# Kernel tuning notes

Measured on AMD Instinct MI355X. Metric: run time of the kernel, lower is better.

The kernel has to match this reference:

```python
import jax, jax.numpy as jnp
import numpy as np

HEADS, DIM_HEAD, BITS = 12, 64, 4


def quantize(q, bits):
    # per-tensor affine fake-quant, exactly as the torch quantize()
    s = (q.max() - q.min()) / (2.0 ** bits - 1.0)
    z = jnp.round(2.0 ** bits - 1.0 - q.max() / s)
    return jnp.round(q / s + z), s, z


def setup_inputs() -> dict:
    key = jax.random.key(0)
    k1, k2, k3, k4 = jax.random.split(key, 4)
    return {
        "x": jax.random.normal(k1, (4, 1024, 768), jnp.float32),
        "w_qkv": jax.random.normal(k2, (2304, 768), jnp.float32) * 0.02,  # torch Linear weight [out,in]
        "w_out": jax.random.normal(k3, (768, 768), jnp.float32) * 0.02,
        "b_out": jax.random.normal(k4, (768,), jnp.float32) * 0.02,
    }


def reference(x, w_qkv, w_out, b_out):
    scale = DIM_HEAD ** -0.5
    B, N, D = x.shape
    # --- quantized QKV projection: x @ W^T with zero-point correction ---
    xq, sx1, zx1 = quantize(x, BITS)
    w1, sw1, zw1 = quantize(w_qkv.T, BITS)  # [D, 3*inner]
    xqkv = (xq @ w1
            - w1.sum(0, keepdims=True) * zx1
            - xq.sum(2, keepdims=True) * zw1
            + zx1 * zw1 * D) * (sx1 * sw1)  # [B, N, 3*inner]
    q, k, v = jnp.split(xqkv, 3, axis=-1)
    to_heads = lambda t: t.reshape(B, N, HEADS, DIM_HEAD).transpose(0, 2, 1, 3)  # b h n d
    q, k, v = to_heads(q), to_heads(k), to_heads(v)
    # --- quantized QK^T (note: original omits the +zq*zk*d term) ---
    qq, sq, zq = quantize(q, BITS)
    kq, sk, zk = quantize(k.transpose(0, 1, 3, 2), BITS)  # b h d n
    dots = (qq @ kq
            - kq.sum(2, keepdims=True) * zq
            - qq.sum(3, keepdims=True) * zk) * (scale * sq * sk)  # b h n n
    a = jax.nn.softmax(dots, axis=-1)
    # --- quantized A @ V ---
    aq, sa, za = quantize(a, BITS)
    vq, sv, zv = quantize(v, BITS)
    out = (aq @ vq
           - vq.sum(2, keepdims=True) * za
           - aq.sum(3, keepdims=True) * zv
           + za * zv * N) * (sa * sv)  # b h n d
    out = out.transpose(0, 2, 1, 3).reshape(B, N, HEADS * DIM_HEAD)
    # --- quantized output projection (faithful to original: correction uses
    # xqkv.sum / xqkv width, reproducing the source's use of `x` here) ---
    oq, sx2, zx2 = quantize(out, BITS)
    w2, sw2, zw2 = quantize(w_out.T, BITS)  # [inner, D]
    o = (oq @ w2
         - w2.sum(0, keepdims=True) * zx2
         - xqkv.sum(2, keepdims=True) * zw2
         + zx2 * zw2 * xqkv.shape[2]) * (sx2 * sw2) + b_out
    return o
```

## Files before the change

kernel.cpp:

```cpp
#include <hip/hip_runtime.h>
#include <math.h>

#define HEADS 12
#define DH    64
#define Dm    768
#define I3    2304
#define Nn    1024
#define Mm    4096
#define BHt   48
#define LOG2E 1.4426950408889634f

#define P_X  0
#define P_W1 1
#define P_Q  2
#define P_K  3
#define P_V  4
#define P_A  5
#define P_O  6
#define P_W2 7

typedef int   v4i __attribute__((ext_vector_type(4)));
typedef float v4f __attribute__((ext_vector_type(4)));

#if __has_builtin(__builtin_amdgcn_exp2f)
#define EXP2(x) __builtin_amdgcn_exp2f(x)
#else
#define EXP2(x) exp2f(x)
#endif

__device__ inline unsigned encf(float f) {
    unsigned u = __float_as_uint(f);
    return (u & 0x80000000u) ? ~u : (u | 0x80000000u);
}
__device__ inline float decf(unsigned u) {
    return (u & 0x80000000u) ? __uint_as_float(u & 0x7fffffffu) : __uint_as_float(~u);
}
__device__ inline void get_sz(const unsigned* scal, int pair, float* s, float* z) {
    float mn = decf(scal[2 * pair]);
    float mx = decf(scal[2 * pair + 1]);
    float ss = (mx - mn) / 15.0f;
    *s = ss;
    *z = rintf(15.0f - mx / ss);
}

__device__ inline void swz_bh(int blk, int* bh, int* itile) {
    int xcd = blk & 7, idx = blk >> 3;
    *itile = idx & 15;
    *bh = xcd + 8 * (idx >> 4);
}

__global__ __launch_bounds__(256) void k_init(unsigned* scal, float* z1, int n1, float* z2, int n2) {
    int g = blockIdx.x * 256 + threadIdx.x;
    if (g < n1) z1[g] = 0.f;
    if (g < n2) z2[g] = 0.f;
    if (g < 8) { scal[2 * g] = 0xFFFFFFFFu; scal[2 * g + 1] = 0u; }
}

__global__ __launch_bounds__(256) void k_minmax3(const float* x, const float* w1, const float* w2,
                                                 unsigned* scal) {
    __shared__ float rmn[256], rmx[256];
    int bid = blockIdx.x, tid = threadIdx.x;
    const float* src; int rows, pair, b0, nb;
    if (bid < 256)      { src = x;  rows = 4096; pair = P_X;  b0 = 0;   nb = 256; }
    else if (bid < 384) { src = w1; rows = 2304; pair = P_W1; b0 = 256; nb = 128; }
    else                { src = w2; rows = 768;  pair = P_W2; b0 = 384; nb = 64;  }
    float mn = INFINITY, mx = -INFINITY;
    for (int r = bid - b0; r < rows; r += nb) {
        const float* row = src + (long)r * 768;
#pragma unroll
        for (int k = 0; k < 3; ++k) {
            float v = row[tid + k * 256];
            mn = fminf(mn, v); mx = fmaxf(mx, v);
        }
    }
    rmn[tid] = mn; rmx[tid] = mx; __syncthreads();
    for (int s = 128; s > 0; s >>= 1) {
        if (tid < s) { rmn[tid] = fminf(rmn[tid], rmn[tid + s]); rmx[tid] = fmaxf(rmx[tid], rmx[tid + s]); }
        __syncthreads();
    }
    if (tid == 0) {
        atomicMin(&scal[2 * pair], encf(rmn[0]));
        atomicMax(&scal[2 * pair + 1], encf(rmx[0]));
    }
}

__global__ __launch_bounds__(256) void k_quant3(const float* x, const float* w1, const float* w2,
                                                const unsigned* scal,
                                                signed char* xq, signed char* wq, signed char* w2q,
                                                float* rs_x, float* rs_w1, float* rs_w2) {
    __shared__ float red[256];
    int bid = blockIdx.x, tid = threadIdx.x;
    const float* src; signed char* dq; float* rs; int pair, r;
    if (bid < 4096)      { src = x;  dq = xq;  rs = rs_x;  pair = P_X;  r = bid; }
    else if (bid < 6400) { src = w1; dq = wq;  rs = rs_w1; pair = P_W1; r = bid - 4096; }
    else                 { src = w2; dq = w2q; rs = rs_w2; pair = P_W2; r = bid - 6400; }
    float s, z; get_sz(scal, pair, &s, &z);
    const float* row = src + (long)r * 768;
    signed char* drow = dq + (long)r * 768;
    float acc = 0.f;
#pragma unroll
    for (int k = 0; k < 3; ++k) {
        int c = tid + k * 256;
        float q = rintf(row[c] / s + z);
        drow[c] = (signed char)(int)q;
        acc += q;
    }
    red[tid] = acc; __syncthreads();
    for (int s2 = 128; s2 > 0; s2 >>= 1) { if (tid < s2) red[tid] += red[tid + s2]; __syncthreads(); }
    if (tid == 0) rs[r] = red[0];
}

__global__ __launch_bounds__(256) void k_quant_rows(const float* src, const unsigned* scal, int pair,
                                                    signed char* dq) {
    int r = blockIdx.x, tid = threadIdx.x;
    float s, z; get_sz(scal, pair, &s, &z);
    const float* row = src + (long)r * 768;
    signed char* drow = dq + (long)r * 768;
#pragma unroll
    for (int k = 0; k < 3; ++k) {
        int c = tid + k * 256;
        float q = rintf(row[c] / s + z);
        drow[c] = (signed char)(int)q;
    }
}

__global__ __launch_bounds__(256) void k_gemm_mfma(const signed char* A, const signed char* B,
                                                   const float* colsumB, const float* rowsumA,
                                                   const float* bias, float* C, int K, int ldC,
                                                   const unsigned* scal, int pairA, int pairB,
                                                   float corrK, int do_stats, float* rowsum_out,
                                                   unsigned* scal_mm) {
    __shared__ __align__(16) signed char As[128 * 64];
    __shared__ __align__(16) signed char Bs[128 * 64];
    __shared__ float red[256];
    int tid = threadIdx.x;
    int wave = tid >> 6, lane = tid & 63;
    int col16 = lane & 15, quad = lane >> 4;
    long rowbase = (long)blockIdx.y * 128;
    long colbase = (long)blockIdx.x * 128;

    int c4 = tid & 3, r4 = tid >> 2;
    const signed char* ag0 = A + (rowbase + r4) * K + c4 * 16;
    const signed char* ag1 = A + (rowbase + r4 + 64) * K + c4 * 16;
    const signed char* bg0 = B + (colbase + r4) * K + c4 * 16;
    const signed char* bg1 = B + (colbase + r4 + 64) * K + c4 * 16;
    int soff0 = ((r4 >> 4) << 10) + (c4 << 8) + ((r4 & 15) << 4);
    int soff1 = soff0 + 4096;

    v4i ra0 = *(const v4i*)ag0;
    v4i ra1 = *(const v4i*)ag1;
    v4i rb0 = *(const v4i*)bg0;
    v4i rb1 = *(const v4i*)bg1;

    const int afrag_off = wave * 2048 + quad * 256 + col16 * 16;
    const int bfrag_off = quad * 256 + col16 * 16;
    v4i acc[2][8] = {};
    int nk = K >> 6;
    for (int kt = 0; kt < nk; ++kt) {
        *(v4i*)(As + soff0) = ra0;
        *(v4i*)(As + soff1) = ra1;
        *(v4i*)(Bs + soff0) = rb0;
        *(v4i*)(Bs + soff1) = rb1;
        __syncthreads();
        if (kt + 1 < nk) {
            int ko = (kt + 1) << 6;
            ra0 = *(const v4i*)(ag0 + ko);
            ra1 = *(const v4i*)(ag1 + ko);
            rb0 = *(const v4i*)(bg0 + ko);
            rb1 = *(const v4i*)(bg1 + ko);
        }
        v4i af0 = *(const v4i*)(As + afrag_off);
        v4i af1 = *(const v4i*)(As + afrag_off + 1024);
        v4i bf[8];
#pragma unroll
        for (int g = 0; g < 8; ++g) bf[g] = *(const v4i*)(Bs + bfrag_off + g * 1024);
#pragma unroll
        for (int g = 0; g < 8; ++g) {
            acc[0][g] = __builtin_amdgcn_mfma_i32_16x16x64_i8(af0, bf[g], acc[0][g], 0, 0, 0);
            acc[1][g] = __builtin_amdgcn_mfma_i32_16x16x64_i8(af1, bf[g], acc[1][g], 0, 0, 0);
        }
        __syncthreads();
    }

    float sA, zA, sB, zB;
    get_sz(scal, pairA, &sA, &zA);
    get_sz(scal, pairB, &sB, &zB);
    float sAB = sA * sB;
    float zz = (zA * zB) * corrK;
    float vmn = INFINITY, vmx = -INFINITY;
    float rowpart[2][4] = {};
#pragma unroll
    for (int i2 = 0; i2 < 2; ++i2)
#pragma unroll
        for (int g = 0; g < 8; ++g) {
            long col = colbase + g * 16 + col16;
            float cs = colsumB[col] * zA;
            float bv = bias ? bias[col] : 0.f;
#pragma unroll
            for (int r = 0; r < 4; ++r) {
                long row = rowbase + wave * 32 + i2 * 16 + quad * 4 + r;
                float v = ((float)acc[i2][g][r] - cs - rowsumA[row] * zB + zz) * sAB + bv;
                C[row * ldC + col] = v;
                rowpart[i2][r] += v;
                vmn = fminf(vmn, v); vmx = fmaxf(vmx, v);
            }
        }
    if (do_stats) {
#pragma unroll
        for (int i2 = 0; i2 < 2; ++i2)
#pragma unroll
            for (int r = 0; r < 4; ++r) {
                float s = rowpart[i2][r];
                s += __shfl_xor(s, 1); s += __shfl_xor(s, 2);
                s += __shfl_xor(s, 4); s += __shfl_xor(s, 8);
                if (col16 == 0)
                    atomicAdd(&rowsum_out[rowbase + wave * 32 + i2 * 16 + quad * 4 + r], s);
            }
        int pair = P_Q + (int)(colbase / 768);
        red[tid] = vmx; __syncthreads();
        for (int s = 128; s > 0; s >>= 1) { if (tid < s) red[tid] = fmaxf(red[tid], red[tid + s]); __syncthreads(); }
        if (tid == 0) atomicMax(&scal_mm[2 * pair + 1], encf(red[0]));
        __syncthreads();
        red[tid] = vmn; __syncthreads();
        for (int s = 128; s > 0; s >>= 1) { if (tid < s) red[tid] = fminf(red[tid], red[tid + s]); __syncthreads(); }
        if (tid == 0) atomicMin(&scal_mm[2 * pair], encf(red[0]));
    }
}

__global__ __launch_bounds__(256) void k_quant_qkv2(const float* xqkv, const unsigned* scal,
                                                    signed char* qq, signed char* kq, signed char* vqT,
                                                    float* rowsum_qq, float* cskc, float* colsum_vq) {
    __shared__ __align__(16) signed char vt[64 * 80];
    __shared__ float vred[4][64];
    int blk = blockIdx.x;
    int bh = blk >> 4, itile = blk & 15;
    int tid = threadIdx.x;
    int wave = tid >> 6, d = tid & 63;
    int b = bh / HEADS, h = bh - HEADS * b;
    float sq, zq, sk, zk, sv, zv;
    get_sz(scal, P_Q, &sq, &zq);
    get_sz(scal, P_K, &sk, &zk);
    get_sz(scal, P_V, &sv, &zv);
    float zqcsc2 = zq * ((0.125f * sq) * sk) * LOG2E;
    int vb = 0;
    float vsum = 0.f;
    for (int ir = 0; ir < 16; ++ir) {
        int il = wave * 16 + ir;
        int i = itile * 64 + il;
        const float* row = xqkv + ((long)b * Nn + i) * I3 + h * DH;
        float q = rintf(row[d] / sq + zq);
        float k = rintf(row[768 + d] / sk + zk);
        float v = rintf(row[1536 + d] / sv + zv);
        long o = ((long)bh * Nn + i) * 64 + d;
        qq[o] = (signed char)(int)q;
        kq[o] = (signed char)(int)k;
        vsum += v;
        vb |= ((int)v & 0xff) << ((ir & 3) * 8);
        if ((ir & 3) == 3) {
            *(int*)(vt + d * 80 + (il & ~3)) = vb;
            vb = 0;
        }
        float s1 = q, s2 = k;
        for (int off = 32; off > 0; off >>= 1) {
            s1 += __shfl_down(s1, off);
            s2 += __shfl_down(s2, off);
        }
        if (d == 0) { rowsum_qq[bh * Nn + i] = s1; cskc[bh * Nn + i] = s2 * zqcsc2; }
    }
    vred[wave][d] = vsum;
    __syncthreads();
    int dd = tid >> 2, c = tid & 3;
    *(v4i*)(vqT + ((long)bh * 64 + dd) * 1024 + itile * 64 + c * 16) = *(const v4i*)(vt + dd * 80 + c * 16);
    if (tid < 64)
        atomicAdd(&colsum_vq[bh * 64 + tid],
                  ((vred[0][tid] + vred[1][tid]) + vred[2][tid]) + vred[3][tid]);
}

__global__ __launch_bounds__(256) void k_attn_a8(const signed char* qq, const signed char* kq,
                                                 const float* rowsum_qq, const float* cskc,
                                                 unsigned* scal, float* rowmax, float* sumexp) {
    __shared__ float red[256];
    int bh, itile;
    swz_bh(blockIdx.x, &bh, &itile);
    int tid = threadIdx.x;
    int wave = tid >> 6, lane = tid & 63;
    int col16 = lane & 15, quad = lane >> 4;
    int rowbase = itile * 64 + wave * 16;
    const signed char* kbase = kq + (long)bh * Nn * 64;
    v4i qfrag = *(const v4i*)(qq + ((long)bh * Nn + rowbase + col16) * 64 + quad * 16);
    float sq, zq, sk, zk;
    get_sz(scal, P_Q, &sq, &zq);
    get_sz(scal, P_K, &sk, &zk);
    float csc2 = ((0.125f * sq) * sk) * LOG2E;
    int irow = bh * Nn + rowbase + col16;
    float roff = rowsum_qq[irow] * zk * csc2;
    v4i zero = {0, 0, 0, 0};
    float m[4]    = {-INFINITY, -INFINITY, -INFINITY, -INFINITY};
    float se[4]   = {0.f, 0.f, 0.f, 0.f};
    float lmin[4] = {INFINITY, INFINITY, INFINITY, INFINITY};
    const signed char* kf = kbase + (long)col16 * 64 + quad * 16;
    const float* ckq = cskc + bh * Nn + quad * 4;
    v4i kb[2][4];
#pragma unroll
    for (int t = 0; t < 4; ++t)
        kb[0][t] = *(const v4i*)(kf + (long)(t * 16) * 64);
#pragma unroll 2
    for (int ch = 0; ch < 16; ++ch) {
        int cur = ch & 1, nxt = cur ^ 1;
        int pch = (ch < 15) ? ch + 1 : 15;
#pragma unroll
        for (int t = 0; t < 4; ++t)
            kb[nxt][t] = *(const v4i*)(kf + (long)(pch * 64 + t * 16) * 64);
#pragma unroll
        for (int s = 0; s < 4; ++s) {
            v4i d = __builtin_amdgcn_mfma_i32_16x16x64_i8(kb[cur][s], qfrag, zero, 0, 0, 0);
            v4f ck4 = *(const v4f*)(ckq + ch * 64 + s * 16);
#pragma unroll
            for (int r = 0; r < 4; ++r) {
                float dv = fmaf((float)d[r], csc2, -(ck4[r] + roff));
                lmin[r] = fminf(lmin[r], dv);
                float mn = fmaxf(m[r], dv);
                float e = EXP2(fminf(m[r], dv) - mn);
                se[r] = (dv > m[r]) ? fmaf(se[r], e, 1.0f) : (se[r] + e);
                m[r] = mn;
            }
        }
    }
    float mm = fmaxf(fmaxf(m[0], m[1]), fmaxf(m[2], m[3]));
    float seT = fmaf(se[0], EXP2(m[0] - mm),
               fmaf(se[1], EXP2(m[1] - mm),
               fmaf(se[2], EXP2(m[2] - mm), se[3] * EXP2(m[3] - mm))));
    float lmT = fminf(fminf(lmin[0], lmin[1]), fminf(lmin[2], lmin[3]));
#pragma unroll
    for (int off = 16; off <= 32; off <<= 1) {
        float mo = __shfl_xor(mm, off);
        float so = __shfl_xor(seT, off);
        float lo = __shfl_xor(lmT, off);
        float mn = fmaxf(mm, mo);
        seT = fmaf(seT, EXP2(mm - mn), so * EXP2(mo - mn));
        mm = mn;
        lmT = fminf(lmT, lo);
    }
    if (quad == 0) {
        rowmax[irow] = mm;
        sumexp[irow] = seT;
    }
    float amax_c = 1.0f / seT;
    float amin_c = EXP2(lmT - mm) / seT;
    red[tid] = amax_c; __syncthreads();
    for (int s = 128; s > 0; s >>= 1) { if (tid < s) red[tid] = fmaxf(red[tid], red[tid + s]); __syncthreads(); }
    if (tid == 0) atomicMax(&scal[2 * P_A + 1], encf(red[0]));
    __syncthreads();
    red[tid] = amin_c; __syncthreads();
    for (int s = 128; s > 0; s >>= 1) { if (tid < s) red[tid] = fminf(red[tid], red[tid + s]); __syncthreads(); }
    if (tid == 0) atomicMin(&scal[2 * P_A], encf(red[0]));
}

__global__ __launch_bounds__(256) void k_attn_b8(const signed char* qq, const signed char* kq,
                                                 const signed char* vqT, const float* rowsum_qq,
                                                 const float* cskc, const float* colsum_vq,
                                                 const float* rowmax, const float* sumexp,
                                                 unsigned* scal, float* out_mat) {
    __shared__ __align__(16) signed char AqB[8192];
    __shared__ float red[256];
    int bh, itile;
    swz_bh(blockIdx.x, &bh, &itile);
    int tid = threadIdx.x;
    int wave = tid >> 6, lane = tid & 63;
    int col16 = lane & 15, quad = lane >> 4;
    int rowbase = itile * 64 + wave * 16;
    int b = bh / HEADS, h = bh - HEADS * b;
    const signed char* kbase = kq + (long)bh * Nn * 64;
    const signed char* vbase = vqT + (long)bh * 64 * 1024;
    v4i qfrag = *(const v4i*)(qq + ((long)bh * Nn + rowbase + col16) * 64 + quad * 16);
    float sq, zq, sk, zk, sv, zv, sa, za;
    get_sz(scal, P_Q, &sq, &zq);
    get_sz(scal, P_K, &sk, &zk);
    get_sz(scal, P_V, &sv, &zv);
    get_sz(scal, P_A, &sa, &za);
    float csc2 = ((0.125f * sq) * sk) * LOG2E;
    int irow = bh * Nn + rowbase + col16;
    float roff = rowsum_qq[irow] * zk * csc2 + rowmax[irow];
    float crcp = 1.0f / (sumexp[irow] * sa);
    v4i accPV[4] = {};
    float rs_a = 0.f;
    v4i zero = {0, 0, 0, 0};
    const signed char* kf = kbase + (long)col16 * 64 + quad * 16;
    const float* ckq = cskc + bh * Nn + quad * 4;
    const int wbase = wave * 1024 + col16 * 16 + quad * 4;
    const int rbase = wave * 1024 + quad * 256 + col16 * 16;

    v4i kb0[4], kb1[4];
#pragma unroll
    for (int t = 0; t < 4; ++t) {
        kb0[t] = *(const v4i*)(kf + (long)(t * 16) * 64);
        kb1[t] = *(const v4i*)(kf + (long)(64 + t * 16) * 64);
    }

#define QUANT_CHUNK(CH, BUF, KB)                                                        \
    {                                                                                   \
        _Pragma("unroll")                                                               \
        for (int s = 0; s < 4; ++s) {                                                   \
            v4i d = __builtin_amdgcn_mfma_i32_16x16x64_i8(KB[s], qfrag, zero, 0, 0, 0); \
            v4f ck4 = *(const v4f*)(ckq + (CH) * 64 + s * 16);                          \
            unsigned pks = 0;                                                           \
            _Pragma("unroll")                                                           \
            for (int r = 0; r < 4; ++r) {                                               \
                float es = fmaf((float)d[r], csc2, -(ck4[r] + roff));                   \
                float aqv = rintf(fmaf(EXP2(es), crcp, za));                            \
                rs_a += aqv;                                                            \
                pks |= ((unsigned)(int)aqv & 255u) << (8 * r);                          \
            }                                                                           \
            *(int*)(AqB + (BUF) * 4096 + wbase + s * 256) = (int)pks;                   \
        }                                                                               \
    }

#define BODY(CH, CUR, KBc, KBn)                                                         \
    {                                                                                   \
        v4i pa = *(const v4i*)(AqB + (CUR) * 4096 + rbase);                             \
        v4i bv[4];                                                                      \
        _Pragma("unroll")                                                               \
        for (int g = 0; g < 4; ++g)                                                     \
            bv[g] = *(const v4i*)(vbase + (long)(g * 16 + col16) * 1024 + (CH) * 64 + quad * 16); \
        if ((CH) < 14) {                                                                \
            _Pragma("unroll")                                                           \
            for (int t = 0; t < 4; ++t)                                                 \
                KBc[t] = *(const v4i*)(kf + (long)(((CH) + 2) * 64 + t * 16) * 64);     \
        }                                                                               \
        if ((CH) < 15) QUANT_CHUNK((CH) + 1, 1 - (CUR), KBn)                            \
        _Pragma("unroll")                                                               \
        for (int g = 0; g < 4; ++g)                                                     \
            accPV[g] = __builtin_amdgcn_mfma_i32_16x16x64_i8(bv[g], pa, accPV[g], 0, 0, 0); \
    }

    QUANT_CHUNK(0, 0, kb0)
    for (int ch2 = 0; ch2 < 8; ++ch2) {
        int ch = ch2 * 2;
        BODY(ch, 0, kb0, kb1)
        BODY(ch + 1, 1, kb1, kb0)
    }
#undef BODY
#undef QUANT_CHUNK

    rs_a += __shfl_xor(rs_a, 16);
    rs_a += __shfl_xor(rs_a, 32);

    float sav = sa * sv;
    float zz = (za * zv) * 1024.0f;
    float vmn = INFINITY, vmx = -INFINITY;
    long obase = ((long)b * Nn + rowbase + col16) * Dm + h * DH;
#pragma unroll
    for (int g = 0; g < 4; ++g) {
        int d4 = g * 16 + quad * 4;
        v4f cs4 = *(const v4f*)(colsum_vq + bh * 64 + d4);
        v4f ov;
#pragma unroll
        for (int rr = 0; rr < 4; ++rr) {
            float v = ((float)accPV[g][rr] - cs4[rr] * za - rs_a * zv + zz) * sav;
            ov[rr] = v;
            vmn = fminf(vmn, v); vmx = fmaxf(vmx, v);
        }
        *(v4f*)(out_mat + obase + d4) = ov;
    }
    red[tid] = vmx; __syncthreads();
    for (int s = 128; s > 0; s >>= 1) { if (tid < s) red[tid] = fmaxf(red[tid], red[tid + s]); __syncthreads(); }
    if (tid == 0) atomicMax(&scal[2 * P_O + 1], encf(red[0]));
    __syncthreads();
    red[tid] = vmn; __syncthreads();
    for (int s = 128; s > 0; s >>= 1) { if (tid < s) red[tid] = fminf(red[tid], red[tid + s]); __syncthreads(); }
    if (tid == 0) atomicMin(&scal[2 * P_O], encf(red[0]));
}

extern "C" void kernel_launch(void* const* d_in, const int* in_sizes, int n_in,
                              void* d_out, int out_size, void* d_ws, size_t ws_size,
                              hipStream_t stream) {
    const float* x     = (const float*)d_in[0];
    const float* w_qkv = (const float*)d_in[1];
    const float* w_out = (const float*)d_in[2];
    const float* b_out = (const float*)d_in[3];

    char* ws = (char*)d_ws;
    size_t off = 0;
    auto alloc = [&](size_t n) -> char* {
        char* p = ws + off;
        off = (off + n + 255) & ~(size_t)255;
        return p;
    };
    unsigned*    scal        = (unsigned*)alloc(64);
    float*       xqkv        = (float*)alloc((size_t)Mm * I3 * 4);
    float*       out_mat     = (float*)alloc((size_t)Mm * Dm * 4);
    signed char* xq          = (signed char*)alloc((size_t)Mm * Dm);
    signed char* wq          = (signed char*)alloc((size_t)I3 * Dm);
    signed char* w2q         = (signed char*)alloc((size_t)Dm * Dm);
    signed char* oq          = (signed char*)alloc((size_t)Mm * Dm);
    signed char* qq          = (signed char*)alloc((size_t)BHt * Nn * DH);
    signed char* kq          = (signed char*)alloc((size_t)BHt * Nn * DH);
    signed char* vqT         = (signed char*)alloc((size_t)BHt * Nn * DH);
    float*       rowsum_xq   = (float*)alloc((size_t)Mm * 4);
    float*       colsum_w1   = (float*)alloc((size_t)I3 * 4);
    float*       colsum_w2   = (float*)alloc((size_t)Dm * 4);
    float*       rowsum_xqkv = (float*)alloc((size_t)Mm * 4);
    float*       rowsum_qq   = (float*)alloc((size_t)BHt * Nn * 4);
    float*       cskc        = (float*)alloc((size_t)BHt * Nn * 4);
    float*       colsum_vq   = (float*)alloc((size_t)BHt * DH * 4);
    float*       rowmax      = (float*)alloc((size_t)BHt * Nn * 4);
    float*       sumexp      = (float*)alloc((size_t)BHt * Nn * 4);

    k_init<<<28, 256, 0, stream>>>(scal, rowsum_xqkv, Mm, colsum_vq, BHt * DH);

    k_minmax3<<<448, 256, 0, stream>>>(x, w_qkv, w_out, scal);
    k_quant3<<<7168, 256, 0, stream>>>(x, w_qkv, w_out, scal, xq, wq, w2q,
                                       rowsum_xq, colsum_w1, colsum_w2);

    {
        dim3 g(I3 / 128, Mm / 128);
        k_gemm_mfma<<<g, 256, 0, stream>>>(xq, wq, colsum_w1, rowsum_xq, nullptr, xqkv,
                                           Dm, I3, scal, P_X, P_W1, 768.0f,
                                           1, rowsum_xqkv, scal);
    }

    k_quant_qkv2<<<BHt * 16, 256, 0, stream>>>(xqkv, scal, qq, kq, vqT,
                                               rowsum_qq, cskc, colsum_vq);

    k_attn_a8<<<BHt * 16, 256, 0, stream>>>(qq, kq, rowsum_qq, cskc, scal, rowmax, sumexp);
    k_attn_b8<<<BHt * 16, 256, 0, stream>>>(qq, kq, vqT, rowsum_qq, cskc, colsum_vq,
                                            rowmax, sumexp, scal, out_mat);

    k_quant_rows<<<Mm, 256, 0, stream>>>(out_mat, scal, P_O, oq);

    {
        dim3 g(Dm / 128, Mm / 128);
        k_gemm_mfma<<<g, 256, 0, stream>>>(oq, w2q, colsum_w2, rowsum_xqkv, b_out, (float*)d_out,
                                           Dm, Dm, scal, P_O, P_W2, 2304.0f,
                                           0, nullptr, nullptr);
    }
}
```

Before: 261.6 us.

## Split attention key range across wave pairs and double the grid

Both attention kernels now cover 32 query rows per block instead of 64. Each pair of waves splits the 1024 keys into two halves, and the partial softmax statistics (max, sum-exp, min) and partial PV accumulators are merged through shared memory. The launch grid doubles to 1536 blocks, giving more parallelism and shorter per-wave loops across the CUs. In exchange it adds extra syncthreads and LDS merge traffic, and each Q fragment is loaded by twice as many blocks.

```diff
diff --git a/kernel.cpp b/kernel.cpp
--- a/kernel.cpp
+++ b/kernel.cpp
@@ -43,10 +43,10 @@
     *z = rintf(15.0f - mx / ss);
 }
 
-__device__ inline void swz_bh(int blk, int* bh, int* itile) {
+__device__ inline void swz_bh32(int blk, int* bh, int* itile) {
     int xcd = blk & 7, idx = blk >> 3;
-    *itile = idx & 15;
-    *bh = xcd + 8 * (idx >> 4);
+    *itile = idx & 31;
+    *bh = xcd + 8 * (idx >> 5);
 }
 
 __global__ __launch_bounds__(256) void k_init(unsigned* scal, float* z1, int n1, float* z2, int n2) {
@@ -280,12 +280,15 @@
                                                  const float* rowsum_qq, const float* cskc,
                                                  unsigned* scal, float* rowmax, float* sumexp) {
     __shared__ float red[256];
+    __shared__ float Mj[2][64], Sj[2][64], Lj[2][64];
     int bh, itile;
-    swz_bh(blockIdx.x, &bh, &itile);
+    swz_bh32(blockIdx.x, &bh, &itile);
     int tid = threadIdx.x;
     int wave = tid >> 6, lane = tid & 63;
     int col16 = lane & 15, quad = lane >> 4;
-    int rowbase = itile * 64 + wave * 16;
+    int rowbase = itile * 32 + (wave >> 1) * 16;
+    int jhalf = wave & 1;
+    int c0 = jhalf * 8;
     const signed char* kbase = kq + (long)bh * Nn * 64;
     v4i qfrag = *(const v4i*)(qq + ((long)bh * Nn + rowbase + col16) * 64 + quad * 16);
     float sq, zq, sk, zk;
@@ -298,16 +301,16 @@
     float m[4]    = {-INFINITY, -INFINITY, -INFINITY, -INFINITY};
     float se[4]   = {0.f, 0.f, 0.f, 0.f};
     float lmin[4] = {INFINITY, INFINITY, INFINITY, INFINITY};
-    const signed char* kf = kbase + (long)col16 * 64 + quad * 16;
-    const float* ckq = cskc + bh * Nn + quad * 4;
+    const signed char* kf = kbase + (long)(c0 * 64 + col16) * 64 + quad * 16;
+    const float* ckq = cskc + bh * Nn + c0 * 64 + quad * 4;
     v4i kb[2][4];
 #pragma unroll
     for (int t = 0; t < 4; ++t)
         kb[0][t] = *(const v4i*)(kf + (long)(t * 16) * 64);
 #pragma unroll 2
-    for (int ch = 0; ch < 16; ++ch) {
+    for (int ch = 0; ch < 8; ++ch) {
         int cur = ch & 1, nxt = cur ^ 1;
-        int pch = (ch < 15) ? ch + 1 : 15;
+        int pch = (ch < 7) ? ch + 1 : 7;
 #pragma unroll
         for (int t = 0; t < 4; ++t)
             kb[nxt][t] = *(const v4i*)(kf + (long)(pch * 64 + t * 16) * 64);
@@ -341,12 +344,23 @@
         mm = mn;
         lmT = fminf(lmT, lo);
     }
-    if (quad == 0) {
-        rowmax[irow] = mm;
-        sumexp[irow] = seT;
-    }
-    float amax_c = 1.0f / seT;
-    float amin_c = EXP2(lmT - mm) / seT;
+    if (jhalf) { Mj[wave >> 1][lane] = mm; Sj[wave >> 1][lane] = seT; Lj[wave >> 1][lane] = lmT; }
+    __syncthreads();
+    float amax_c = -INFINITY, amin_c = INFINITY;
+    if (!jhalf) {
+        int p = wave >> 1;
+        float m2 = Mj[p][lane], s2 = Sj[p][lane], l2 = Lj[p][lane];
+        float mn = fmaxf(mm, m2);
+        seT = fmaf(seT, EXP2(mm - mn), s2 * EXP2(m2 - mn));
+        mm = mn;
+        lmT = fminf(lmT, l2);
+        if (quad == 0) {
+            rowmax[irow] = mm;
+            sumexp[irow] = seT;
+        }
+        amax_c = 1.0f / seT;
+        amin_c = EXP2(lmT - mm) / seT;
+    }
     red[tid] = amax_c; __syncthreads();
     for (int s = 128; s > 0; s >>= 1) { if (tid < s) red[tid] = fmaxf(red[tid], red[tid + s]); __syncthreads(); }
     if (tid == 0) atomicMax(&scal[2 * P_A + 1], encf(red[0]));
@@ -364,14 +378,15 @@
     __shared__ __align__(16) signed char AqB[8192];
     __shared__ float red[256];
     int bh, itile;
-    swz_bh(blockIdx.x, &bh, &itile);
+    swz_bh32(blockIdx.x, &bh, &itile);
     int tid = threadIdx.x;
     int wave = tid >> 6, lane = tid & 63;
     int col16 = lane & 15, quad = lane >> 4;
-    int rowbase = itile * 64 + wave * 16;
+    int rowbase = itile * 32 + (wave >> 1) * 16;
+    int jhalf = wave & 1;
+    int c0 = jhalf * 8;
     int b = bh / HEADS, h = bh - HEADS * b;
     const signed char* kbase = kq + (long)bh * Nn * 64;
-    const signed char* vbase = vqT + (long)bh * 64 * 1024;
     v4i qfrag = *(const v4i*)(qq + ((long)bh * Nn + rowbase + col16) * 64 + quad * 16);
     float sq, zq, sk, zk, sv, zv, sa, za;
     get_sz(scal, P_Q, &sq, &zq);
@@ -385,8 +400,9 @@
     v4i accPV[4] = {};
     float rs_a = 0.f;
     v4i zero = {0, 0, 0, 0};
-    const signed char* kf = kbase + (long)col16 * 64 + quad * 16;
-    const float* ckq = cskc + bh * Nn + quad * 4;
+    const signed char* kf = kbase + (long)(c0 * 64 + col16) * 64 + quad * 16;
+    const float* ckq = cskc + bh * Nn + c0 * 64 + quad * 4;
+    const signed char* vbase = vqT + (long)bh * 64 * 1024 + c0 * 64;
     const int wbase = wave * 1024 + col16 * 16 + quad * 4;
     const int rbase = wave * 1024 + quad * 256 + col16 * 16;
 
@@ -422,19 +438,19 @@
         _Pragma("unroll")                                                               \
         for (int g = 0; g < 4; ++g)                                                     \
             bv[g] = *(const v4i*)(vbase + (long)(g * 16 + col16) * 1024 + (CH) * 64 + quad * 16); \
-        if ((CH) < 14) {                                                                \
+        if ((CH) < 6) {                                                                 \
             _Pragma("unroll")                                                           \
             for (int t = 0; t < 4; ++t)                                                 \
                 KBc[t] = *(const v4i*)(kf + (long)(((CH) + 2) * 64 + t * 16) * 64);     \
         }                                                                               \
-        if ((CH) < 15) QUANT_CHUNK((CH) + 1, 1 - (CUR), KBn)                            \
+        if ((CH) < 7) QUANT_CHUNK((CH) + 1, 1 - (CUR), KBn)                             \
         _Pragma("unroll")                                                               \
         for (int g = 0; g < 4; ++g)                                                     \
             accPV[g] = __builtin_amdgcn_mfma_i32_16x16x64_i8(bv[g], pa, accPV[g], 0, 0, 0); \
     }
 
     QUANT_CHUNK(0, 0, kb0)
-    for (int ch2 = 0; ch2 < 8; ++ch2) {
+    for (int ch2 = 0; ch2 < 4; ++ch2) {
         int ch = ch2 * 2;
         BODY(ch, 0, kb0, kb1)
         BODY(ch + 1, 1, kb1, kb0)
@@ -445,23 +461,43 @@
     rs_a += __shfl_xor(rs_a, 16);
     rs_a += __shfl_xor(rs_a, 32);
 
-    float sav = sa * sv;
-    float zz = (za * zv) * 1024.0f;
+    __syncthreads();
+    if (jhalf) {
+        int p = wave >> 1;
+#pragma unroll
+        for (int g = 0; g < 4; ++g)
+            *(v4i*)(AqB + p * 4096 + g * 1024 + lane * 16) = accPV[g];
+        red[p * 64 + lane] = rs_a;
+    }
+    __syncthreads();
     float vmn = INFINITY, vmx = -INFINITY;
-    long obase = ((long)b * Nn + rowbase + col16) * Dm + h * DH;
-#pragma unroll
-    for (int g = 0; g < 4; ++g) {
-        int d4 = g * 16 + quad * 4;
-        v4f cs4 = *(const v4f*)(colsum_vq + bh * 64 + d4);
-        v4f ov;
-#pragma unroll
-        for (int rr = 0; rr < 4; ++rr) {
-            float v = ((float)accPV[g][rr] - cs4[rr] * za - rs_a * zv + zz) * sav;
-            ov[rr] = v;
-            vmn = fminf(vmn, v); vmx = fmaxf(vmx, v);
-        }
-        *(v4f*)(out_mat + obase + d4) = ov;
-    }
+    if (!jhalf) {
+        int p = wave >> 1;
+#pragma unroll
+        for (int g = 0; g < 4; ++g) {
+            v4i o = *(const v4i*)(AqB + p * 4096 + g * 1024 + lane * 16);
+            accPV[g] += o;
+        }
+        rs_a += red[p * 64 + lane];
+
+        float sav = sa * sv;
+        float zz = (za * zv) * 1024.0f;
+        long obase = ((long)b * Nn + rowbase + col16) * Dm + h * DH;
+#pragma unroll
+        for (int g = 0; g < 4; ++g) {
+            int d4 = g * 16 + quad * 4;
+            v4f cs4 = *(const v4f*)(colsum_vq + bh * 64 + d4);
+            v4f ov;
+#pragma unroll
+            for (int rr = 0; rr < 4; ++rr) {
+                float v = ((float)accPV[g][rr] - cs4[rr] * za - rs_a * zv + zz) * sav;
+                ov[rr] = v;
+                vmn = fminf(vmn, v); vmx = fmaxf(vmx, v);
+            }
+            *(v4f*)(out_mat + obase + d4) = ov;
+        }
+    }
+    __syncthreads();
     red[tid] = vmx; __syncthreads();
     for (int s = 128; s > 0; s >>= 1) { if (tid < s) red[tid] = fmaxf(red[tid], red[tid + s]); __syncthreads(); }
     if (tid == 0) atomicMax(&scal[2 * P_O + 1], encf(red[0]));
@@ -522,8 +558,8 @@
     k_quant_qkv2<<<BHt * 16, 256, 0, stream>>>(xqkv, scal, qq, kq, vqT,
                                                rowsum_qq, cskc, colsum_vq);
 
-    k_attn_a8<<<BHt * 16, 256, 0, stream>>>(qq, kq, rowsum_qq, cskc, scal, rowmax, sumexp);
-    k_attn_b8<<<BHt * 16, 256, 0, stream>>>(qq, kq, vqT, rowsum_qq, cskc, colsum_vq,
+    k_attn_a8<<<BHt * 32, 256, 0, stream>>>(qq, kq, rowsum_qq, cskc, scal, rowmax, sumexp);
+    k_attn_b8<<<BHt * 32, 256, 0, stream>>>(qq, kq, vqT, rowsum_qq, cskc, colsum_vq,
                                             rowmax, sumexp, scal, out_mat);
 
     k_quant_rows<<<Mm, 256, 0, stream>>>(out_mat, scal, P_O, oq);
```

Measured after the change: 285.1 us. +9.0%, slower.
